# Performance work log

Measured on AMD Instinct MI355X. Metric: run time of the kernel, lower is better.

Reference implementation:

```python
import jax, jax.numpy as jnp
import numpy as np

DIM = 192
HEADS = 4
EMBED = 48


def setup_inputs() -> dict:
    key = jax.random.key(0)
    ks = jax.random.split(key, 8)
    b, c, h, w = 8, DIM, 128, 128
    x = jax.random.normal(ks[0], (b, c, h, w), dtype=jnp.float32)
    prior = jax.random.normal(ks[1], (b, 1, EMBED * 4), dtype=jnp.float32)
    # learned params (bias=False)
    w_qkv = jax.random.normal(ks[2], (3 * c, c), dtype=jnp.float32) * (1.0 / np.sqrt(c))
    w_dw = jax.random.normal(ks[3], (3 * c, 1, 3, 3), dtype=jnp.float32) * (1.0 / 3.0)
    w_proj = jax.random.normal(ks[4], (c, c), dtype=jnp.float32) * (1.0 / np.sqrt(c))
    w_kernel = jax.random.normal(ks[5], (2 * c, EMBED * 4), dtype=jnp.float32) * (1.0 / np.sqrt(EMBED * 4))
    temperature = jnp.ones((HEADS, 1, 1), dtype=jnp.float32)
    return {"x": x, "prior": prior, "w_qkv": w_qkv, "w_dw": w_dw,
            "w_proj": w_proj, "w_kernel": w_kernel, "temperature": temperature}


def _mdta(x, prior, w_qkv, w_dw, w_proj, w_kernel, temperature):
    b, c, h, w = x.shape
    # prior modulation: Linear(4*embed -> 2*dim), broadcast over (h,w)
    kv = jnp.einsum('blf,of->blo', prior, w_kernel)[:, 0]        # (b, 2c)
    kv1, kv2 = kv[:, :c], kv[:, c:]
    x = x * kv1[:, :, None, None] + kv2[:, :, None, None]
    # 1x1 conv -> depthwise 3x3 conv
    qkv = jnp.einsum('bchw,oc->bohw', x, w_qkv)                   # (b, 3c, h, w)
    qkv = jax.lax.conv_general_dilated(
        qkv, w_dw, window_strides=(1, 1), padding='SAME',
        dimension_numbers=('NCHW', 'OIHW', 'NCHW'), feature_group_count=3 * c)
    q, k, v = jnp.split(qkv, 3, axis=1)
    ch = c // HEADS
    def heads(t):  # (b, c, h, w) -> (b, head, ch, h*w)
        return t.reshape(b, HEADS, ch, h * w)
    q, k, v = heads(q), heads(k), heads(v)
    # L2 normalize over the (h w) reduction axis
    q = q / jnp.linalg.norm(q, axis=-1, keepdims=True).clip(1e-12)
    k = k / jnp.linalg.norm(k, axis=-1, keepdims=True).clip(1e-12)
    attn = jnp.einsum('bhcn,bhdn->bhcd', q, k) * temperature      # (b, head, ch, ch)
    attn = jax.nn.softmax(attn, axis=-1)
    out = jnp.einsum('bhcd,bhdn->bhcn', attn, v).reshape(b, c, h, w)
    return jnp.einsum('bchw,oc->bohw', out, w_proj)


def reference(x, prior, w_qkv, w_dw, w_proj, w_kernel, temperature):
    return _mdta(x, prior, w_qkv, w_dw, w_proj, w_kernel, temperature)
```

## Files before the change

kernel.cpp:

```cpp
#include <hip/hip_runtime.h>
#include <hip/hip_bf16.h>
#include <stdint.h>

typedef float f32x4 __attribute__((ext_vector_type(4)));
typedef __bf16 bf16x8 __attribute__((ext_vector_type(8)));
typedef __bf16 bf16x4 __attribute__((ext_vector_type(4)));
typedef __bf16 bf16x2 __attribute__((ext_vector_type(2)));

#define NB 8
#define NC 192
#define NO 576
#define NH 128
#define NWID 128
#define NSP 16384
#define NHEADS 4
#define NCH 48

#define OFF_KV    0u
#define OFF_SSQ   12288u
#define OFF_S     24576u
#define OFF_WB    319488u
#define OFF_M     540672u
#define OFF_XT    1130496u
#define OFF_QKV1  152125440u

#define GR(r) (((r) ^ ((r) >> 2)) & 7)

__device__ __forceinline__ void g2l16(const void* g, void* l) {
    __builtin_amdgcn_global_load_lds((const __attribute__((address_space(1))) void*)g,
                                     (__attribute__((address_space(3))) void*)l, 16, 0, 0);
}

__global__ void k_prep(const float* __restrict__ prior, const float* __restrict__ w_kernel,
                       const float* __restrict__ w_qkv, float* __restrict__ kv,
                       float* __restrict__ zbase, __bf16* __restrict__ Wb) {
    int t = blockIdx.x * 256 + threadIdx.x;
    if (t < 76800) zbase[t] = 0.f;
    if (t < NO * NC) Wb[t] = (__bf16)w_qkv[t];
    if (t < NB * 384) {
        int b = t / 384, j = t % 384;
        const float* p = prior + b * NC;
        const float* wk = w_kernel + j * NC;
        float s = 0.f;
        for (int f = 0; f < NC; ++f) s += p[f] * wk[f];
        kv[t] = s;
    }
}

__global__ __launch_bounds__(256) void k_xt(const float* __restrict__ x, const float* __restrict__ kv,
                                            __bf16* __restrict__ xt) {
    int b = blockIdx.y;
    int n0 = blockIdx.x * 128;
    __shared__ __align__(16) __bf16 lds[128 * 192];
    int t = threadIdx.x;
    for (int p = 0; p < 24; ++p) {
        int id = p * 256 + t;
        int c = id >> 5, n4 = (id & 31) << 2;
        f32x4 v = *reinterpret_cast<const f32x4*>(x + (size_t)(b * NC + c) * NSP + n0 + n4);
        float k1 = kv[b * 384 + c], k2 = kv[b * 384 + 192 + c];
        int chi = (c >> 3) ^ ((n4 >> 2) & 7);
        int base = chi * 16 + (c & 7) * 2;
#pragma unroll
        for (int j = 0; j < 4; ++j)
            *reinterpret_cast<__bf16*>((char*)lds + (n4 + j) * 384 + base) = (__bf16)(v[j] * k1 + k2);
    }
    __syncthreads();
    for (int p = 0; p < 12; ++p) {
        int id = p * 256 + t;
        int n = id / 24, k = id % 24;
        bf16x8 r = *reinterpret_cast<const bf16x8*>((char*)lds + n * 384 + ((k ^ ((n >> 2) & 7)) << 4));
        *reinterpret_cast<bf16x8*>(xt + (size_t)(b * NSP + n0 + n) * NC + k * 8) = r;
    }
}

__global__ __launch_bounds__(256, 2) void k_qkv(const __bf16* __restrict__ xt, const __bf16* __restrict__ Wb,
                                                __bf16* __restrict__ qkv1) {
    __shared__ __align__(16) char lds[73728];
    int b = blockIdx.y, n0 = blockIdx.x * 128;
    int t = threadIdx.x;
    const __bf16* bsrc = xt + (size_t)(b * NSP + n0) * NC;
#pragma unroll
    for (int i = 0; i < 12; ++i) {
        int s = i * 256 + t;
        int r = s / 24, c = s % 24, g = c ^ (r & 7);
        g2l16(bsrc + (size_t)r * NC + g * 8, lds + s * 16);
    }
#pragma unroll
    for (int i = 0; i < 6; ++i) {
        int s = i * 256 + t;
        int r = s / 24, c = s % 24, g = c ^ (r & 7);
        g2l16(Wb + (size_t)r * NC + g * 8, lds + 49152 + s * 16);
    }
    asm volatile("s_waitcnt vmcnt(0)" ::: "memory");
    __syncthreads();
    int w = t >> 6, l = t & 63, lr = l & 15, lg = l >> 4;
    bf16x8 bgf[6][2];
#pragma unroll
    for (int ks = 0; ks < 6; ++ks) {
        int c16 = ks * 4 + lg;
#pragma unroll
        for (int nf = 0; nf < 2; ++nf) {
            int r = w * 32 + nf * 16 + lr;
            bgf[ks][nf] = *reinterpret_cast<const bf16x8*>(lds + r * 384 + ((c16 ^ (r & 7)) << 4));
        }
    }
    for (int ot = 0; ot < 9; ++ot) {
        f32x4 acc[4][2] = {};
#pragma unroll
        for (int ks = 0; ks < 6; ++ks) {
            int c16 = ks * 4 + lg;
            bf16x8 a[4];
#pragma unroll
            for (int mf = 0; mf < 4; ++mf) {
                int r = mf * 16 + lr;
                a[mf] = *reinterpret_cast<const bf16x8*>(lds + 49152 + r * 384 + ((c16 ^ (r & 7)) << 4));
            }
#pragma unroll
            for (int mf = 0; mf < 4; ++mf)
#pragma unroll
                for (int nf = 0; nf < 2; ++nf)
                    acc[mf][nf] = __builtin_amdgcn_mfma_f32_16x16x32_bf16(a[mf], bgf[ks][nf], acc[mf][nf], 0, 0, 0);
        }
        __syncthreads();
        if (ot < 8) {
            const __bf16* asrc = Wb + (size_t)(ot + 1) * 64 * NC;
#pragma unroll
            for (int i = 0; i < 6; ++i) {
                int s = i * 256 + t;
                int r = s / 24, c = s % 24, g = c ^ (r & 7);
                g2l16(asrc + (size_t)r * NC + g * 8, lds + 49152 + s * 16);
            }
        }
        int o0 = ot * 64;
#pragma unroll
        for (int mf = 0; mf < 4; ++mf)
#pragma unroll
            for (int rr = 0; rr < 4; ++rr) {
                int orow = o0 + mf * 16 + lg * 4 + rr;
#pragma unroll
                for (int nf = 0; nf < 2; ++nf)
                    qkv1[(size_t)(b * NO + orow) * NSP + n0 + w * 32 + nf * 16 + lr] = (__bf16)acc[mf][nf][rr];
            }
        if (ot < 8) {
            asm volatile("s_waitcnt vmcnt(32)" ::: "memory");
            __syncthreads();
        }
    }
}

__global__ __launch_bounds__(256) void k_dw(const __bf16* __restrict__ qkv1, const float* __restrict__ w_dw,
                                            __bf16* __restrict__ qkv2, float* __restrict__ ssq) {
    int task = blockIdx.x * 4 + (threadIdx.x >> 6);
    int l = threadIdx.x & 63;
    int strip = task & 7;
    int bo = task >> 3;
    int o = bo % NO, b = bo / NO;
    const __bf16* src = qkv1 + (size_t)bo * NSP;
    __bf16* dst = qkv2 + (size_t)bo * NSP;
    float wd[9];
#pragma unroll
    for (int i = 0; i < 9; ++i) wd[i] = w_dw[o * 9 + i];
    int ys = strip * 16;
    float a0, b0, L0, R0, a1, b1, L1, R1, a2, b2, L2, R2;

#define LOADROW(Y, A, B, L_, R_) {                                            \
        bf16x2 p = {};                                                        \
        int y_ = (Y);                                                         \
        if (y_ >= 0 && y_ < NH) p = *reinterpret_cast<const bf16x2*>(src + y_ * NWID + 2 * l); \
        A = (float)p[0]; B = (float)p[1];                                     \
        L_ = __shfl(B, l - 1); R_ = __shfl(A, l + 1);                         \
        if (l == 0) L_ = 0.f;                                                 \
        if (l == 63) R_ = 0.f; }

    LOADROW(ys - 1, a0, b0, L0, R0)
    LOADROW(ys,     a1, b1, L1, R1)
    float ss = 0.f;
    bool qk = (o < 384);
#pragma unroll 4
    for (int i = 0; i < 16; ++i) {
        LOADROW(ys + i + 1, a2, b2, L2, R2)
        float oa = L0 * wd[0] + a0 * wd[1] + b0 * wd[2]
                 + L1 * wd[3] + a1 * wd[4] + b1 * wd[5]
                 + L2 * wd[6] + a2 * wd[7] + b2 * wd[8];
        float ob = a0 * wd[0] + b0 * wd[1] + R0 * wd[2]
                 + a1 * wd[3] + b1 * wd[4] + R1 * wd[5]
                 + a2 * wd[6] + b2 * wd[7] + R2 * wd[8];
        bf16x2 ov; ov[0] = (__bf16)oa; ov[1] = (__bf16)ob;
        *reinterpret_cast<bf16x2*>(dst + (ys + i) * NWID + 2 * l) = ov;
        if (qk) { float fa = (float)ov[0], fb = (float)ov[1]; ss += fa * fa + fb * fb; }
        a0 = a1; b0 = b1; L0 = L1; R0 = R1;
        a1 = a2; b1 = b2; L1 = L2; R1 = R2;
    }
#undef LOADROW
    if (qk) {
        for (int off = 32; off > 0; off >>= 1) ss += __shfl_down(ss, off);
        if (l == 0) atomicAdd(&ssq[b * 384 + o], ss);
    }
}

__global__ __launch_bounds__(256, 3) void k_sdot(const __bf16* __restrict__ qkv2, float* __restrict__ S) {
    __shared__ __align__(16) char lds[49152];
    int b = blockIdx.z, h = blockIdx.y, n0 = blockIdx.x * 512;
    int t = threadIdx.x;
    int w = t >> 6, l = t & 63, lr = l & 15, lg = l >> 4;
    const __bf16* qsrc = qkv2 + (size_t)(b * NO + h * NCH) * NSP + n0;
    const __bf16* ksrc = qkv2 + (size_t)(b * NO + 192 + h * NCH) * NSP + n0;
    f32x4 acc[3][3] = {};
    for (int pass = 0; pass < 2; ++pass) {
        if (pass) __syncthreads();
        int coff = pass * 256;
#pragma unroll
        for (int i = 0; i < 6; ++i) {
            int s = i * 256 + t;
            int r = s >> 5, c = s & 31, g = c ^ (r & 7);
            g2l16(qsrc + (size_t)r * NSP + coff + g * 8, lds + s * 16);
        }
#pragma unroll
        for (int i = 0; i < 6; ++i) {
            int s = i * 256 + t;
            int r = s >> 5, c = s & 31, g = c ^ (r & 7);
            g2l16(ksrc + (size_t)r * NSP + coff + g * 8, lds + 24576 + s * 16);
        }
        asm volatile("s_waitcnt vmcnt(0)" ::: "memory");
        __syncthreads();
#pragma unroll
        for (int j = 0; j < 2; ++j) {
            int c16 = (w * 2 + j) * 4 + lg;
            bf16x8 a[3], bb[3];
#pragma unroll
            for (int mf = 0; mf < 3; ++mf) {
                int r = mf * 16 + lr;
                a[mf] = *reinterpret_cast<const bf16x8*>(lds + r * 512 + ((c16 ^ (r & 7)) << 4));
            }
#pragma unroll
            for (int nf = 0; nf < 3; ++nf) {
                int r = nf * 16 + lr;
                bb[nf] = *reinterpret_cast<const bf16x8*>(lds + 24576 + r * 512 + ((c16 ^ (r & 7)) << 4));
            }
#pragma unroll
            for (int mf = 0; mf < 3; ++mf)
#pragma unroll
                for (int nf = 0; nf < 3; ++nf)
                    acc[mf][nf] = __builtin_amdgcn_mfma_f32_16x16x32_bf16(a[mf], bb[nf], acc[mf][nf], 0, 0, 0);
        }
    }
    __syncthreads();
    float* red = (float*)lds;
#pragma unroll
    for (int mf = 0; mf < 3; ++mf)
#pragma unroll
        for (int nf = 0; nf < 3; ++nf)
#pragma unroll
            for (int r = 0; r < 4; ++r) {
                int c = mf * 16 + lg * 4 + r, d = nf * 16 + lr;
                red[(w * 48 + c) * 49 + d] = acc[mf][nf][r];
            }
    __syncthreads();
    float* Sb = S + (size_t)(b * NHEADS + h) * NCH * NCH;
    for (int i = 0; i < 9; ++i) {
        int idx = t + i * 256;
        int c = idx / 48, d = idx % 48;
        float s = red[c * 49 + d] + red[(48 + c) * 49 + d] + red[(96 + c) * 49 + d] + red[(144 + c) * 49 + d];
        atomicAdd(&Sb[c * 48 + d], s);
    }
}

__global__ __launch_bounds__(256) void k_soft(const float* __restrict__ S, const float* __restrict__ ssq,
                                              const float* __restrict__ temp, const float* __restrict__ w_proj,
                                              __bf16* __restrict__ M) {
    int b = blockIdx.x / NHEADS, h = blockIdx.x % NHEADS;
    int tid = threadIdx.x;
    __shared__ float attn[48][48];
    __shared__ float inv[96];
    if (tid < 96) {
        int c = tid % 48;
        int isK = tid / 48;
        float v = ssq[b * 384 + isK * 192 + h * NCH + c];
        float nrm = fmaxf(sqrtf(v), 1e-12f);
        inv[tid] = 1.f / nrm;
    }
    __syncthreads();
    float tp = temp[h];
    const float* Sb = S + (size_t)(b * NHEADS + h) * NCH * NCH;
    for (int i = 0; i < 9; ++i) {
        int idx = tid + i * 256;
        int c = idx / 48, d = idx % 48;
        attn[c][d] = Sb[c * 48 + d] * inv[c] * inv[48 + d] * tp;
    }
    __syncthreads();
    if (tid < 48) {
        float m = -1e30f;
        for (int d = 0; d < 48; ++d) m = fmaxf(m, attn[tid][d]);
        float sum = 0.f;
        for (int d = 0; d < 48; ++d) { float e = __expf(attn[tid][d] - m); attn[tid][d] = e; sum += e; }
        float r = 1.f / sum;
        for (int d = 0; d < 48; ++d) attn[tid][d] *= r;
    }
    __syncthreads();
    for (int i = 0; i < 36; ++i) {
        int idx = tid + i * 256;
        int oo = idx / 48, d = idx % 48;
        const float* wp = w_proj + oo * NC + h * NCH;
        float s = 0.f;
        for (int c = 0; c < 48; ++c) s += wp[c] * attn[c][d];
        M[(size_t)(b * NC + oo) * NC + h * NCH + d] = (__bf16)s;
    }
}

__global__ __launch_bounds__(256, 2) void k_out(const __bf16* __restrict__ Mw, const __bf16* __restrict__ qkv2,
                                                float* __restrict__ outp) {
    __shared__ __align__(16) char lds[73728];
    int b = blockIdx.y, n0 = blockIdx.x * 128;
    int t = threadIdx.x;
    const __bf16* asrc0 = Mw + (size_t)(b * NC) * NC;
#pragma unroll
    for (int i = 0; i < 6; ++i) {
        int s = i * 256 + t;
        int r = s / 24, c = s % 24, g = c ^ GR(r);
        g2l16(asrc0 + (size_t)r * NC + g * 8, lds + 49152 + s * 16);
    }
    const __bf16* vb = qkv2 + (size_t)(b * NO + 384) * NSP + n0;
#pragma unroll 4
    for (int p = 0; p < 24; ++p) {
        int id = p * 256 + t;
        int c = id >> 5, n4 = (id & 31) << 2;
        bf16x4 vv = *reinterpret_cast<const bf16x4*>(vb + (size_t)c * NSP + n4);
#pragma unroll
        for (int j = 0; j < 4; ++j) {
            int n = n4 + j;
            int chi = (c >> 3) ^ GR(n);
            *reinterpret_cast<__bf16*>((char*)lds + n * 384 + chi * 16 + (c & 7) * 2) = vv[j];
        }
    }
    asm volatile("s_waitcnt vmcnt(0)" ::: "memory");
    __syncthreads();
    int w = t >> 6, l = t & 63, lr = l & 15, lg = l >> 4;
    bf16x8 bgf[6][2];
#pragma unroll
    for (int ks = 0; ks < 6; ++ks) {
        int c16 = ks * 4 + lg;
#pragma unroll
        for (int nf = 0; nf < 2; ++nf) {
            int r = w * 32 + nf * 16 + lr;
            bgf[ks][nf] = *reinterpret_cast<const bf16x8*>(lds + r * 384 + ((c16 ^ GR(r)) << 4));
        }
    }
    for (int ot = 0; ot < 3; ++ot) {
        f32x4 acc[4][2] = {};
#pragma unroll
        for (int ks = 0; ks < 6; ++ks) {
            int c16 = ks * 4 + lg;
            bf16x8 a[4];
#pragma unroll
            for (int mf = 0; mf < 4; ++mf) {
                int r = mf * 16 + lr;
                a[mf] = *reinterpret_cast<const bf16x8*>(lds + 49152 + r * 384 + ((c16 ^ GR(r)) << 4));
            }
#pragma unroll
            for (int mf = 0; mf < 4; ++mf)
#pragma unroll
                for (int nf = 0; nf < 2; ++nf)
                    acc[mf][nf] = __builtin_amdgcn_mfma_f32_16x16x32_bf16(a[mf], bgf[ks][nf], acc[mf][nf], 0, 0, 0);
        }
        __syncthreads();
        if (ot < 2) {
            const __bf16* asrc = Mw + (size_t)(b * NC + (ot + 1) * 64) * NC;
#pragma unroll
            for (int i = 0; i < 6; ++i) {
                int s = i * 256 + t;
                int r = s / 24, c = s % 24, g = c ^ GR(r);
                g2l16(asrc + (size_t)r * NC + g * 8, lds + 49152 + s * 16);
            }
        }
        int o0 = ot * 64;
#pragma unroll
        for (int mf = 0; mf < 4; ++mf)
#pragma unroll
            for (int rr = 0; rr < 4; ++rr) {
                int orow = o0 + mf * 16 + lg * 4 + rr;
#pragma unroll
                for (int nf = 0; nf < 2; ++nf)
                    outp[(size_t)(b * NC + orow) * NSP + n0 + w * 32 + nf * 16 + lr] = acc[mf][nf][rr];
            }
        if (ot < 2) {
            asm volatile("s_waitcnt vmcnt(32)" ::: "memory");
            __syncthreads();
        }
    }
}

extern "C" void kernel_launch(void* const* d_in, const int* in_sizes, int n_in,
                              void* d_out, int out_size, void* d_ws, size_t ws_size,
                              hipStream_t stream) {
    const float* x        = (const float*)d_in[0];
    const float* prior    = (const float*)d_in[1];
    const float* w_qkv    = (const float*)d_in[2];
    const float* w_dw     = (const float*)d_in[3];
    const float* w_proj   = (const float*)d_in[4];
    const float* w_kernel = (const float*)d_in[5];
    const float* temp     = (const float*)d_in[6];
    char* ws = (char*)d_ws;
    float*  kv    = (float*)(ws + OFF_KV);
    float*  ssq   = (float*)(ws + OFF_SSQ);
    float*  S     = (float*)(ws + OFF_S);
    __bf16* Wb    = (__bf16*)(ws + OFF_WB);
    __bf16* M     = (__bf16*)(ws + OFF_M);
    __bf16* xt    = (__bf16*)(ws + OFF_XT);
    __bf16* qkv2  = (__bf16*)(ws + OFF_XT);
    __bf16* qkv1  = (__bf16*)(ws + OFF_QKV1);
    float*  outp  = (float*)d_out;

    k_prep<<<432, 256, 0, stream>>>(prior, w_kernel, w_qkv, kv, (float*)(ws + OFF_SSQ), Wb);
    k_xt<<<dim3(128, 8), 256, 0, stream>>>(x, kv, xt);
    k_qkv<<<dim3(128, 8), 256, 0, stream>>>(xt, Wb, qkv1);
    k_dw<<<9216, 256, 0, stream>>>(qkv1, w_dw, qkv2, ssq);
    k_sdot<<<dim3(32, 4, 8), 256, 0, stream>>>(qkv2, S);
    k_soft<<<32, 256, 0, stream>>>(S, ssq, temp, w_proj, M);
    k_out<<<dim3(128, 8), 256, 0, stream>>>(M, qkv2, outp);
}
```

Before: 225.4 us.

## Fuse depthwise conv for q/k into S-dot kernel, limit k_dw to v

```diff
diff --git a/kernel.cpp b/kernel.cpp
--- a/kernel.cpp
+++ b/kernel.cpp
@@ -30,6 +30,15 @@
     __builtin_amdgcn_global_load_lds((const __attribute__((address_space(1))) void*)g,
                                      (__attribute__((address_space(3))) void*)l, 16, 0, 0);
 }
+
+#define LOADROW(SRC, Y, A, B, L_, R_) {                                       \
+        bf16x2 p = {};                                                        \
+        int y_ = (Y);                                                         \
+        if (y_ >= 0 && y_ < NH) p = *reinterpret_cast<const bf16x2*>((SRC) + y_ * NWID + 2 * l); \
+        A = (float)p[0]; B = (float)p[1];                                     \
+        L_ = __shfl(B, l - 1); R_ = __shfl(A, l + 1);                         \
+        if (l == 0) L_ = 0.f;                                                 \
+        if (l == 63) R_ = 0.f; }
 
 __global__ void k_prep(const float* __restrict__ prior, const float* __restrict__ w_kernel,
                        const float* __restrict__ w_qkv, float* __restrict__ kv,
@@ -130,6 +139,7 @@
                 int r = s / 24, c = s % 24, g = c ^ (r & 7);
                 g2l16(asrc + (size_t)r * NC + g * 8, lds + 49152 + s * 16);
             }
+            __builtin_amdgcn_sched_barrier(0);
         }
         int o0 = ot * 64;
 #pragma unroll
@@ -149,36 +159,24 @@
 }
 
 __global__ __launch_bounds__(256) void k_dw(const __bf16* __restrict__ qkv1, const float* __restrict__ w_dw,
-                                            __bf16* __restrict__ qkv2, float* __restrict__ ssq) {
+                                            __bf16* __restrict__ qkv2) {
     int task = blockIdx.x * 4 + (threadIdx.x >> 6);
     int l = threadIdx.x & 63;
     int strip = task & 7;
     int bo = task >> 3;
-    int o = bo % NO, b = bo / NO;
-    const __bf16* src = qkv1 + (size_t)bo * NSP;
-    __bf16* dst = qkv2 + (size_t)bo * NSP;
+    int o = 384 + (bo % 192), b = bo / 192;
+    const __bf16* src = qkv1 + (size_t)(b * NO + o) * NSP;
+    __bf16* dst = qkv2 + (size_t)(b * NO + o) * NSP;
     float wd[9];
 #pragma unroll
     for (int i = 0; i < 9; ++i) wd[i] = w_dw[o * 9 + i];
     int ys = strip * 16;
     float a0, b0, L0, R0, a1, b1, L1, R1, a2, b2, L2, R2;
-
-#define LOADROW(Y, A, B, L_, R_) {                                            \
-        bf16x2 p = {};                                                        \
-        int y_ = (Y);                                                         \
-        if (y_ >= 0 && y_ < NH) p = *reinterpret_cast<const bf16x2*>(src + y_ * NWID + 2 * l); \
-        A = (float)p[0]; B = (float)p[1];                                     \
-        L_ = __shfl(B, l - 1); R_ = __shfl(A, l + 1);                         \
-        if (l == 0) L_ = 0.f;                                                 \
-        if (l == 63) R_ = 0.f; }
-
-    LOADROW(ys - 1, a0, b0, L0, R0)
-    LOADROW(ys,     a1, b1, L1, R1)
-    float ss = 0.f;
-    bool qk = (o < 384);
+    LOADROW(src, ys - 1, a0, b0, L0, R0)
+    LOADROW(src, ys,     a1, b1, L1, R1)
 #pragma unroll 4
     for (int i = 0; i < 16; ++i) {
-        LOADROW(ys + i + 1, a2, b2, L2, R2)
+        LOADROW(src, ys + i + 1, a2, b2, L2, R2)
         float oa = L0 * wd[0] + a0 * wd[1] + b0 * wd[2]
                  + L1 * wd[3] + a1 * wd[4] + b1 * wd[5]
                  + L2 * wd[6] + a2 * wd[7] + b2 * wd[8];
@@ -187,62 +185,75 @@
                  + a2 * wd[6] + b2 * wd[7] + R2 * wd[8];
         bf16x2 ov; ov[0] = (__bf16)oa; ov[1] = (__bf16)ob;
         *reinterpret_cast<bf16x2*>(dst + (ys + i) * NWID + 2 * l) = ov;
-        if (qk) { float fa = (float)ov[0], fb = (float)ov[1]; ss += fa * fa + fb * fb; }
         a0 = a1; b0 = b1; L0 = L1; R0 = R1;
         a1 = a2; b1 = b2; L1 = L2; R1 = R2;
     }
-#undef LOADROW
-    if (qk) {
+}
+
+__global__ __launch_bounds__(256, 3) void k_sdot(const __bf16* __restrict__ qkv1, const float* __restrict__ w_dw,
+                                                 float* __restrict__ ssq, float* __restrict__ S) {
+    __shared__ __align__(16) char lds[49152];
+    int b = blockIdx.z, h = blockIdx.y, ct = blockIdx.x;
+    int y0 = ct * 2;
+    int t = threadIdx.x, w = t >> 6, l = t & 63, lr = l & 15, lg = l >> 4;
+    for (int i = 0; i < 24; ++i) {
+        int c = w + 4 * i;
+        int o = (c < 48) ? (h * NCH + c) : (192 + h * NCH + (c - 48));
+        const __bf16* src = qkv1 + (size_t)(b * NO + o) * NSP;
+        float wd[9];
+#pragma unroll
+        for (int k = 0; k < 9; ++k) wd[k] = w_dw[o * 9 + k];
+        float a0, e0, L0, R0, a1, e1, L1, R1, a2, e2, L2, R2, a3, e3, L3, R3;
+        LOADROW(src, y0 - 1, a0, e0, L0, R0)
+        LOADROW(src, y0,     a1, e1, L1, R1)
+        LOADROW(src, y0 + 1, a2, e2, L2, R2)
+        LOADROW(src, y0 + 2, a3, e3, L3, R3)
+        float oa = L0 * wd[0] + a0 * wd[1] + e0 * wd[2]
+                 + L1 * wd[3] + a1 * wd[4] + e1 * wd[5]
+                 + L2 * wd[6] + a2 * wd[7] + e2 * wd[8];
+        float ob = a0 * wd[0] + e0 * wd[1] + R0 * wd[2]
+                 + a1 * wd[3] + e1 * wd[4] + R1 * wd[5]
+                 + a2 * wd[6] + e2 * wd[7] + R2 * wd[8];
+        float oc = L1 * wd[0] + a1 * wd[1] + e1 * wd[2]
+                 + L2 * wd[3] + a2 * wd[4] + e2 * wd[5]
+                 + L3 * wd[6] + a3 * wd[7] + e3 * wd[8];
+        float od = a1 * wd[0] + e1 * wd[1] + R1 * wd[2]
+                 + a2 * wd[3] + e2 * wd[4] + R2 * wd[5]
+                 + a3 * wd[6] + e3 * wd[7] + R3 * wd[8];
+        bf16x2 ov0; ov0[0] = (__bf16)oa; ov0[1] = (__bf16)ob;
+        bf16x2 ov1; ov1[0] = (__bf16)oc; ov1[1] = (__bf16)od;
+        float ss = 0.f;
+        { float f; f = (float)ov0[0]; ss += f * f; f = (float)ov0[1]; ss += f * f;
+          f = (float)ov1[0]; ss += f * f; f = (float)ov1[1]; ss += f * f; }
+        int nl0 = 2 * l;
+        int off0 = (nl0 & 7) * 2;
+        *reinterpret_cast<bf16x2*>(lds + c * 512 + (((nl0 >> 3) ^ (c & 7)) << 4) + off0) = ov0;
+        int nl1 = 128 + 2 * l;
+        *reinterpret_cast<bf16x2*>(lds + c * 512 + (((nl1 >> 3) ^ (c & 7)) << 4) + off0) = ov1;
         for (int off = 32; off > 0; off >>= 1) ss += __shfl_down(ss, off);
         if (l == 0) atomicAdd(&ssq[b * 384 + o], ss);
     }
-}
-
-__global__ __launch_bounds__(256, 3) void k_sdot(const __bf16* __restrict__ qkv2, float* __restrict__ S) {
-    __shared__ __align__(16) char lds[49152];
-    int b = blockIdx.z, h = blockIdx.y, n0 = blockIdx.x * 512;
-    int t = threadIdx.x;
-    int w = t >> 6, l = t & 63, lr = l & 15, lg = l >> 4;
-    const __bf16* qsrc = qkv2 + (size_t)(b * NO + h * NCH) * NSP + n0;
-    const __bf16* ksrc = qkv2 + (size_t)(b * NO + 192 + h * NCH) * NSP + n0;
+    __syncthreads();
     f32x4 acc[3][3] = {};
-    for (int pass = 0; pass < 2; ++pass) {
-        if (pass) __syncthreads();
-        int coff = pass * 256;
-#pragma unroll
-        for (int i = 0; i < 6; ++i) {
-            int s = i * 256 + t;
-            int r = s >> 5, c = s & 31, g = c ^ (r & 7);
-            g2l16(qsrc + (size_t)r * NSP + coff + g * 8, lds + s * 16);
-        }
-#pragma unroll
-        for (int i = 0; i < 6; ++i) {
-            int s = i * 256 + t;
-            int r = s >> 5, c = s & 31, g = c ^ (r & 7);
-            g2l16(ksrc + (size_t)r * NSP + coff + g * 8, lds + 24576 + s * 16);
-        }
-        asm volatile("s_waitcnt vmcnt(0)" ::: "memory");
-        __syncthreads();
-#pragma unroll
-        for (int j = 0; j < 2; ++j) {
-            int c16 = (w * 2 + j) * 4 + lg;
-            bf16x8 a[3], bb[3];
-#pragma unroll
-            for (int mf = 0; mf < 3; ++mf) {
-                int r = mf * 16 + lr;
-                a[mf] = *reinterpret_cast<const bf16x8*>(lds + r * 512 + ((c16 ^ (r & 7)) << 4));
-            }
-#pragma unroll
-            for (int nf = 0; nf < 3; ++nf) {
-                int r = nf * 16 + lr;
-                bb[nf] = *reinterpret_cast<const bf16x8*>(lds + 24576 + r * 512 + ((c16 ^ (r & 7)) << 4));
-            }
-#pragma unroll
-            for (int mf = 0; mf < 3; ++mf)
-#pragma unroll
-                for (int nf = 0; nf < 3; ++nf)
-                    acc[mf][nf] = __builtin_amdgcn_mfma_f32_16x16x32_bf16(a[mf], bb[nf], acc[mf][nf], 0, 0, 0);
-        }
+#pragma unroll
+    for (int j = 0; j < 2; ++j) {
+        int c16 = (w * 2 + j) * 4 + lg;
+        bf16x8 a[3], bb[3];
+#pragma unroll
+        for (int mf = 0; mf < 3; ++mf) {
+            int r = mf * 16 + lr;
+            a[mf] = *reinterpret_cast<const bf16x8*>(lds + r * 512 + ((c16 ^ (r & 7)) << 4));
+        }
+#pragma unroll
+        for (int nf = 0; nf < 3; ++nf) {
+            int r = 48 + nf * 16 + lr;
+            bb[nf] = *reinterpret_cast<const bf16x8*>(lds + r * 512 + ((c16 ^ (r & 7)) << 4));
+        }
+#pragma unroll
+        for (int mf = 0; mf < 3; ++mf)
+#pragma unroll
+            for (int nf = 0; nf < 3; ++nf)
+                acc[mf][nf] = __builtin_amdgcn_mfma_f32_16x16x32_bf16(a[mf], bb[nf], acc[mf][nf], 0, 0, 0);
     }
     __syncthreads();
     float* red = (float*)lds;
@@ -371,6 +382,7 @@
                 int r = s / 24, c = s % 24, g = c ^ GR(r);
                 g2l16(asrc + (size_t)r * NC + g * 8, lds + 49152 + s * 16);
             }
+            __builtin_amdgcn_sched_barrier(0);
         }
         int o0 = ot * 64;
 #pragma unroll
@@ -413,8 +425,8 @@
     k_prep<<<432, 256, 0, stream>>>(prior, w_kernel, w_qkv, kv, (float*)(ws + OFF_SSQ), Wb);
     k_xt<<<dim3(128, 8), 256, 0, stream>>>(x, kv, xt);
     k_qkv<<<dim3(128, 8), 256, 0, stream>>>(xt, Wb, qkv1);
-    k_dw<<<9216, 256, 0, stream>>>(qkv1, w_dw, qkv2, ssq);
-    k_sdot<<<dim3(32, 4, 8), 256, 0, stream>>>(qkv2, S);
+    k_dw<<<3072, 256, 0, stream>>>(qkv1, w_dw, qkv2);
+    k_sdot<<<dim3(64, 4, 8), 256, 0, stream>>>(qkv1, w_dw, ssq, S);
     k_soft<<<32, 256, 0, stream>>>(S, ssq, temp, w_proj, M);
     k_out<<<dim3(128, 8), 256, 0, stream>>>(M, qkv2, outp);
 }
```

New measurement: 334.4 us. 1.48x slower.
